# Kernel optimization log

Hardware: AMD Instinct MI355X
Metric: run time of the kernel (lower is better)

Reference implementation:

```python
import jax, jax.numpy as jnp
import numpy as np

B, S, D, H = 4, 2048, 1024, 16
HEAD = D // H
DENOM = float(np.sqrt(D))  # NOTE: original divides by sqrt(hidden_size), not sqrt(head_size)


def setup_inputs() -> dict:
    key = jax.random.key(0)
    ks = jax.random.split(key, 5)
    scale = 1.0 / np.sqrt(D)
    return {
        "hidden_state": jax.random.normal(ks[0], (B, S, D), dtype=jnp.float32),
        "attention_mask": jnp.ones((B, S), dtype=jnp.int32),  # unused in forward (faithful to source)
        "w_q": jax.random.normal(ks[1], (D, D), dtype=jnp.float32) * scale,
        "w_k": jax.random.normal(ks[2], (D, D), dtype=jnp.float32) * scale,
        "w_v": jax.random.normal(ks[3], (D, D), dtype=jnp.float32) * scale,
        "w_o": jax.random.normal(ks[4], (D, D), dtype=jnp.float32) * scale,
    }


def _split_heads(x):
    # [B, S, D] -> [B, H, S, head]
    b, s, _ = x.shape
    return x.reshape(b, s, H, HEAD).transpose(0, 2, 1, 3)


def reference(hidden_state, attention_mask, w_q, w_k, w_v, w_o):
    # nn.Linear(bias=False): y = x @ W^T with W of shape [out, in]
    q = _split_heads(hidden_state @ w_q.T)  # [B, H, S, head]
    k = _split_heads(hidden_state @ w_k.T)
    v = _split_heads(hidden_state @ w_v.T)
    qk = jnp.einsum("bhqd,bhkd->bhqk", q, k) / DENOM  # scale = 1/sqrt(hidden_size)
    attn = jax.nn.softmax(qk, axis=-1)  # attention_mask is NOT applied (matches source)
    ctx = jnp.einsum("bhqk,bhkd->bhqd", attn, v)  # [B, H, S, head]
    ctx = ctx.transpose(0, 2, 1, 3).reshape(hidden_state.shape[0], hidden_state.shape[1], D)
    return ctx @ w_o.T
```

## Files before the change

kernel.cpp:

```cpp
#include <hip/hip_runtime.h>
#include <hip/hip_bf16.h>
#include <math.h>

typedef __bf16 bf16x8 __attribute__((ext_vector_type(8)));
typedef __bf16 bf16x2 __attribute__((ext_vector_type(2)));
typedef float f32x4 __attribute__((ext_vector_type(4)));
typedef float f32x16 __attribute__((ext_vector_type(16)));
typedef unsigned u32x2v __attribute__((ext_vector_type(2)));
typedef unsigned u32x4v __attribute__((ext_vector_type(4)));
typedef unsigned short u16;

#define QSCALE 0.04508422002778011f

__device__ __forceinline__ u16 f2b(float f) {
  union { float f; unsigned u; } x; x.f = f;
  unsigned r = x.u + 0x7fffu + ((x.u >> 16) & 1u);
  return (u16)(r >> 16);
}

__device__ __forceinline__ unsigned pkbf(float a, float b) {
  bf16x2 t = { (__bf16)a, (__bf16)b };
  return __builtin_bit_cast(unsigned, t);
}

#define GLOAD_LDS16(g, s)                                                      \
  __builtin_amdgcn_global_load_lds(                                            \
      (__attribute__((address_space(1))) void*)(void*)(g),                     \
      (__attribute__((address_space(3))) void*)(s), 16, 0, 0)

__global__ void cast_all_kernel(const float* __restrict__ hs,
                                const float* __restrict__ wq, const float* __restrict__ wk,
                                const float* __restrict__ wv, const float* __restrict__ wo,
                                u16* __restrict__ hsb, u16* __restrict__ wqkv,
                                u16* __restrict__ wob) {
  const int w = blockIdx.y;
  const float* src; u16* dst; int n4; float scale = 1.0f;
  if (w == 0)      { src = hs; dst = hsb;                 n4 = 8192 * 1024 / 4; }
  else if (w == 1) { src = wq; dst = wqkv;                n4 = 1024 * 1024 / 4; scale = QSCALE; }
  else if (w == 2) { src = wk; dst = wqkv + 1024 * 1024;  n4 = 1024 * 1024 / 4; }
  else if (w == 3) { src = wv; dst = wqkv + 2 * 1024 * 1024; n4 = 1024 * 1024 / 4; }
  else             { src = wo; dst = wob;                 n4 = 1024 * 1024 / 4; }
  int i = blockIdx.x * blockDim.x + threadIdx.x;
  int stride = gridDim.x * blockDim.x;
  for (; i < n4; i += stride) {
    float4 v = ((const float4*)src)[i];
    ushort4 o;
    o.x = f2b(v.x * scale); o.y = f2b(v.y * scale);
    o.z = f2b(v.z * scale); o.w = f2b(v.w * scale);
    ((ushort4*)dst)[i] = o;
  }
}

template <int OUT_MODE>
__global__ __launch_bounds__(256) void gemm_nt64(const u16* __restrict__ A,
                                                 const u16* __restrict__ B,
                                                 void* __restrict__ O0,
                                                 u16* __restrict__ Ko,
                                                 u16* __restrict__ Vt,
                                                 int nbx) {
  __shared__ u16 As[128 * 64];
  __shared__ u16 Bs[128 * 64];
  const int tid = threadIdx.x;
  const int wid = tid >> 6, lane = tid & 63;
  const int fr = lane & 15, fg = lane >> 4;
  const int wr = wid >> 1, wc = wid & 1;
  const int id = blockIdx.x;
  const int cpx = gridDim.x >> 3;
  const int swzid = (id & 7) * cpx + (id >> 3);
  const int by = swzid / nbx, bx = swzid % nbx;
  const int m0 = by * 128, n0 = bx * 128;
  const int K = 1024;

  f32x4 acc[4][4] = {};

  for (int kt = 0; kt < K; kt += 64) {
#pragma unroll
    for (int i2 = 0; i2 < 4; ++i2) {
      int c = i2 * 256 + tid;
      int row = c >> 3, sl = c & 7;
      int kc = sl ^ (row & 7);
      GLOAD_LDS16(A + (size_t)(m0 + row) * K + kt + kc * 8, (char*)As + c * 16);
      GLOAD_LDS16(B + (size_t)(n0 + row) * K + kt + kc * 8, (char*)Bs + c * 16);
    }
    __syncthreads();

    bf16x8 af[4][2], bfr[4][2];
#pragma unroll
    for (int m = 0; m < 4; ++m) {
      const int row = wr * 64 + m * 16 + fr;
#pragma unroll
      for (int ks = 0; ks < 2; ++ks)
        af[m][ks] = *(const bf16x8*)((const char*)As + row * 128 +
                                     ((ks * 64 + fg * 16) ^ ((fr & 7) << 4)));
    }
#pragma unroll
    for (int n = 0; n < 4; ++n) {
      const int row = wc * 64 + n * 16 + fr;
#pragma unroll
      for (int ks = 0; ks < 2; ++ks)
        bfr[n][ks] = *(const bf16x8*)((const char*)Bs + row * 128 +
                                      ((ks * 64 + fg * 16) ^ ((fr & 7) << 4)));
    }
    __builtin_amdgcn_s_setprio(1);
#pragma unroll
    for (int m = 0; m < 4; ++m)
#pragma unroll
      for (int n = 0; n < 4; ++n)
#pragma unroll
        for (int ks = 0; ks < 2; ++ks)
          acc[m][n] = __builtin_amdgcn_mfma_f32_16x16x32_bf16(af[m][ks], bfr[n][ks],
                                                              acc[m][n], 0, 0, 0);
    __builtin_amdgcn_s_setprio(0);
    __syncthreads();
  }

#pragma unroll
  for (int m = 0; m < 4; ++m)
#pragma unroll
    for (int n = 0; n < 4; ++n) {
      int gr = m0 + wr * 64 + m * 16 + fg * 4;
      int gc = n0 + wc * 64 + n * 16 + fr;
      if (OUT_MODE == 0) {
#pragma unroll
        for (int j = 0; j < 4; ++j)
          ((float*)O0)[(size_t)(gr + j) * 1024 + gc] = acc[m][n][j];
      } else {
        const int region = n0 >> 10;
        if (region == 2) {
          int vc = gc - 2048;
          int hh = vc >> 6, dd = vc & 63, bb2 = gr >> 11, s0 = gr & 2047;
          ushort4 o;
          o.x = f2b(acc[m][n][0]); o.y = f2b(acc[m][n][1]);
          o.z = f2b(acc[m][n][2]); o.w = f2b(acc[m][n][3]);
          *(ushort4*)(Vt + (((size_t)bb2 * 16 + hh) * 64 + dd) * 2048 + s0) = o;
        } else {
          u16* dst = (region == 0) ? (u16*)O0 : Ko;
          int cc = gc & 1023;
#pragma unroll
          for (int j = 0; j < 4; ++j)
            dst[(size_t)(gr + j) * 1024 + cc] = f2b(acc[m][n][j]);
        }
      }
    }
}

__global__ __launch_bounds__(256, 2) void attn_fwd(const u16* __restrict__ Q,
                                                   const u16* __restrict__ Kg,
                                                   const u16* __restrict__ Vtg,
                                                   u16* __restrict__ O) {
  __shared__ u16 Ks[2][64 * 64];
  __shared__ u16 Vs[2][64 * 64];
  const int tid = threadIdx.x;
  const int wid = tid >> 6, lane = tid & 63;
  const int lq = lane & 31, hi = lane >> 5;
  const int id = blockIdx.x;
  const int swz = (id & 7) * 64 + (id >> 3);
  const int qb = swz & 7, bh = swz >> 3;
  const int b = bh >> 4, h = bh & 15;
  const size_t tokBase = (size_t)b * 2048 * 1024 + h * 64;
  const size_t vBase = (size_t)bh * 64 * 2048;
  const int q0 = qb * 256 + wid * 64;

  bf16x8 qfA[4], qfB[4];
#pragma unroll
  for (int s = 0; s < 4; ++s) {
    qfA[s] = *(const bf16x8*)(Q + tokBase + (size_t)(q0 + lq) * 1024 + s * 16 + hi * 8);
    qfB[s] = *(const bf16x8*)(Q + tokBase + (size_t)(q0 + 32 + lq) * 1024 + s * 16 + hi * 8);
  }

  f32x16 accA0 = {}, accA1 = {}, accB0 = {}, accB1 = {};
  f32x16 lsvA = {}, lsvB = {};

  const int skey = tid >> 3, sdc = tid & 7;
  const int sdg = sdc ^ (skey & 7);
  const int skey2 = (tid + 256) >> 3;
  const int sdg2 = sdc ^ (skey2 & 7);

#define STAGE(bb_, k0_) do {                                                          \
    GLOAD_LDS16(Kg + tokBase + (size_t)((k0_) + skey) * 1024 + sdg * 8,               \
                (char*)Ks[bb_] + tid * 16);                                           \
    GLOAD_LDS16(Kg + tokBase + (size_t)((k0_) + skey2) * 1024 + sdg2 * 8,             \
                (char*)Ks[bb_] + (tid + 256) * 16);                                   \
    GLOAD_LDS16(Vtg + vBase + (size_t)skey * 2048 + (k0_) + sdg * 8,                  \
                (char*)Vs[bb_] + tid * 16);                                           \
    GLOAD_LDS16(Vtg + vBase + (size_t)skey2 * 2048 + (k0_) + sdg2 * 8,                \
                (char*)Vs[bb_] + (tid + 256) * 16);                                   \
  } while (0)

  STAGE(0, 0);
  for (int t = 0; t < 32; ++t) {
    const int bb = t & 1;
    __syncthreads();
    if (t < 31) STAGE(bb ^ 1, (t + 1) * 64);

    f32x16 svA0 = {}, svA1 = {}, svB0 = {}, svB1 = {};
    __builtin_amdgcn_s_setprio(1);
#pragma unroll
    for (int s = 0; s < 4; ++s) {
      bf16x8 kf0 = *(const bf16x8*)((const char*)Ks[bb] + lq * 128 +
                                    ((s * 32 + hi * 16) ^ ((lq & 7) << 4)));
      bf16x8 kf1 = *(const bf16x8*)((const char*)Ks[bb] + (32 + lq) * 128 +
                                    ((s * 32 + hi * 16) ^ ((lq & 7) << 4)));
      svA0 = __builtin_amdgcn_mfma_f32_32x32x16_bf16(kf0, qfA[s], svA0, 0, 0, 0);
      svB0 = __builtin_amdgcn_mfma_f32_32x32x16_bf16(kf0, qfB[s], svB0, 0, 0, 0);
      svA1 = __builtin_amdgcn_mfma_f32_32x32x16_bf16(kf1, qfA[s], svA1, 0, 0, 0);
      svB1 = __builtin_amdgcn_mfma_f32_32x32x16_bf16(kf1, qfB[s], svB1, 0, 0, 0);
    }
    __builtin_amdgcn_s_setprio(0);

#pragma unroll
    for (int i = 0; i < 16; ++i) svA0[i] = __builtin_amdgcn_exp2f(svA0[i]);
#pragma unroll
    for (int i = 0; i < 16; ++i) svA1[i] = __builtin_amdgcn_exp2f(svA1[i]);
#pragma unroll
    for (int i = 0; i < 16; ++i) svB0[i] = __builtin_amdgcn_exp2f(svB0[i]);
#pragma unroll
    for (int i = 0; i < 16; ++i) svB1[i] = __builtin_amdgcn_exp2f(svB1[i]);
    lsvA += svA0; lsvA += svA1;
    lsvB += svB0; lsvB += svB1;

    bf16x8 paA[4], paB[4];
#pragma unroll
    for (int kb = 0; kb < 2; ++kb) {
#pragma unroll
      for (int hh = 0; hh < 2; ++hh) {
        const int rb = hh * 8;
        {
          const f32x16& pv = kb ? svA1 : svA0;
          unsigned w01 = pkbf(pv[rb + 0], pv[rb + 1]);
          unsigned w23 = pkbf(pv[rb + 2], pv[rb + 3]);
          unsigned w45 = pkbf(pv[rb + 4], pv[rb + 5]);
          unsigned w67 = pkbf(pv[rb + 6], pv[rb + 7]);
          u32x2v ra = __builtin_amdgcn_permlane32_swap(w01, w45, false, false);
          u32x2v rc = __builtin_amdgcn_permlane32_swap(w23, w67, false, false);
          u32x4v fw = { ra[0], rc[0], ra[1], rc[1] };
          paA[kb * 2 + hh] = __builtin_bit_cast(bf16x8, fw);
        }
        {
          const f32x16& pv = kb ? svB1 : svB0;
          unsigned w01 = pkbf(pv[rb + 0], pv[rb + 1]);
          unsigned w23 = pkbf(pv[rb + 2], pv[rb + 3]);
          unsigned w45 = pkbf(pv[rb + 4], pv[rb + 5]);
          unsigned w67 = pkbf(pv[rb + 6], pv[rb + 7]);
          u32x2v ra = __builtin_amdgcn_permlane32_swap(w01, w45, false, false);
          u32x2v rc = __builtin_amdgcn_permlane32_swap(w23, w67, false, false);
          u32x4v fw = { ra[0], rc[0], ra[1], rc[1] };
          paB[kb * 2 + hh] = __builtin_bit_cast(bf16x8, fw);
        }
      }
    }

    __builtin_amdgcn_s_setprio(1);
#pragma unroll
    for (int s = 0; s < 4; ++s) {
      bf16x8 bv0 = *(const bf16x8*)((const char*)Vs[bb] + lq * 128 +
                                    ((s * 32 + hi * 16) ^ ((lq & 7) << 4)));
      bf16x8 bv1 = *(const bf16x8*)((const char*)Vs[bb] + (32 + lq) * 128 +
                                    ((s * 32 + hi * 16) ^ ((lq & 7) << 4)));
      accA0 = __builtin_amdgcn_mfma_f32_32x32x16_bf16(paA[s], bv0, accA0, 0, 0, 0);
      accA1 = __builtin_amdgcn_mfma_f32_32x32x16_bf16(paA[s], bv1, accA1, 0, 0, 0);
      accB0 = __builtin_amdgcn_mfma_f32_32x32x16_bf16(paB[s], bv0, accB0, 0, 0, 0);
      accB1 = __builtin_amdgcn_mfma_f32_32x32x16_bf16(paB[s], bv1, accB1, 0, 0, 0);
    }
    __builtin_amdgcn_s_setprio(0);
  }
#undef STAGE

  float totA = 0.f, totB = 0.f;
#pragma unroll
  for (int i = 0; i < 16; ++i) { totA += lsvA[i]; totB += lsvB[i]; }
  totA += __shfl_xor(totA, 32);
  totB += __shfl_xor(totB, 32);
  const float invA = 1.0f / totA, invB = 1.0f / totB;
#pragma unroll
  for (int r = 0; r < 16; ++r) {
    const int q = (r & 3) + 8 * (r >> 2) + 4 * hi;
    const float ivA = __shfl(invA, q);
    const float ivB = __shfl(invB, q);
    const size_t rowA = (size_t)(b * 2048 + q0 + q) * 1024 + h * 64;
    const size_t rowB = (size_t)(b * 2048 + q0 + 32 + q) * 1024 + h * 64;
    O[rowA + lq]      = f2b(accA0[r] * ivA);
    O[rowA + 32 + lq] = f2b(accA1[r] * ivA);
    O[rowB + lq]      = f2b(accB0[r] * ivB);
    O[rowB + 32 + lq] = f2b(accB1[r] * ivB);
  }
}

extern "C" void kernel_launch(void* const* d_in, const int* in_sizes, int n_in,
                              void* d_out, int out_size, void* d_ws, size_t ws_size,
                              hipStream_t stream) {
  const float* hs = (const float*)d_in[0];
  const float* wq = (const float*)d_in[2];
  const float* wk = (const float*)d_in[3];
  const float* wv = (const float*)d_in[4];
  const float* wo = (const float*)d_in[5];

  const size_t TOK = 8192, DD = 1024;
  u16* hsb  = (u16*)d_ws;
  u16* wqkv = hsb + TOK * DD;
  u16* wob  = wqkv + 3 * DD * DD;
  u16* Qb   = wob + DD * DD;
  u16* Kb   = Qb + TOK * DD;
  u16* Vtg  = Kb + TOK * DD;
  u16* Cb   = Vtg + TOK * DD;

  cast_all_kernel<<<dim3(512, 5), 256, 0, stream>>>(hs, wq, wk, wv, wo, hsb, wqkv, wob);

  gemm_nt64<1><<<1536, 256, 0, stream>>>(hsb, wqkv, Qb, Kb, Vtg, 24);

  attn_fwd<<<dim3(512), 256, 0, stream>>>(Qb, Kb, Vtg, Cb);

  gemm_nt64<0><<<512, 256, 0, stream>>>(Cb, wob, d_out, nullptr, nullptr, 8);
}
```

Before: 189.3 us.

## Split attention over key halves with fp32 partials and a reduction kernel

Adds a split-K attention kernel that gives each block half of the key sequence. This doubles the grid to 1024 blocks and raises launch_bounds occupancy to 4, so more of the GPU is filled. Each half writes unnormalized fp32 partial accumulators and row sums to workspace, and a new reduce kernel adds them, normalizes, and writes bf16 context. This works without max-subtraction because the softmax is not max-shifted. The cost is about 64MB of extra fp32 traffic plus one more kernel launch, and the path falls back to the old kernel if the workspace is too small.

```diff
diff --git a/kernel.cpp b/kernel.cpp
--- a/kernel.cpp
+++ b/kernel.cpp
@@ -144,6 +144,82 @@
     }
 }
 
+#define ATTN_TILE_BODY(Kb_, Vb_)                                                      \
+    f32x16 svA0 = {}, svA1 = {}, svB0 = {}, svB1 = {};                                \
+    __builtin_amdgcn_s_setprio(1);                                                    \
+    _Pragma("unroll") for (int s = 0; s < 4; ++s) {                                   \
+      bf16x8 kf0 = *(const bf16x8*)((const char*)(Kb_) + lq * 128 +                   \
+                                    ((s * 32 + hi * 16) ^ ((lq & 7) << 4)));          \
+      bf16x8 kf1 = *(const bf16x8*)((const char*)(Kb_) + (32 + lq) * 128 +            \
+                                    ((s * 32 + hi * 16) ^ ((lq & 7) << 4)));          \
+      svA0 = __builtin_amdgcn_mfma_f32_32x32x16_bf16(kf0, qfA[s], svA0, 0, 0, 0);     \
+      svB0 = __builtin_amdgcn_mfma_f32_32x32x16_bf16(kf0, qfB[s], svB0, 0, 0, 0);     \
+      svA1 = __builtin_amdgcn_mfma_f32_32x32x16_bf16(kf1, qfA[s], svA1, 0, 0, 0);     \
+      svB1 = __builtin_amdgcn_mfma_f32_32x32x16_bf16(kf1, qfB[s], svB1, 0, 0, 0);     \
+    }                                                                                 \
+    __builtin_amdgcn_s_setprio(0);                                                    \
+    _Pragma("unroll") for (int i = 0; i < 16; ++i)                                    \
+      svA0[i] = __builtin_amdgcn_exp2f(svA0[i]);                                      \
+    _Pragma("unroll") for (int i = 0; i < 16; ++i)                                    \
+      svA1[i] = __builtin_amdgcn_exp2f(svA1[i]);                                      \
+    _Pragma("unroll") for (int i = 0; i < 16; ++i)                                    \
+      svB0[i] = __builtin_amdgcn_exp2f(svB0[i]);                                      \
+    _Pragma("unroll") for (int i = 0; i < 16; ++i)                                    \
+      svB1[i] = __builtin_amdgcn_exp2f(svB1[i]);                                      \
+    lsvA += svA0; lsvA += svA1;                                                       \
+    lsvB += svB0; lsvB += svB1;                                                       \
+    bf16x8 paA[4], paB[4];                                                            \
+    _Pragma("unroll") for (int kb = 0; kb < 2; ++kb) {                                \
+      _Pragma("unroll") for (int hh = 0; hh < 2; ++hh) {                              \
+        const int rb = hh * 8;                                                        \
+        {                                                                             \
+          const f32x16& pv = kb ? svA1 : svA0;                                        \
+          unsigned w01 = pkbf(pv[rb + 0], pv[rb + 1]);                                \
+          unsigned w23 = pkbf(pv[rb + 2], pv[rb + 3]);                                \
+          unsigned w45 = pkbf(pv[rb + 4], pv[rb + 5]);                                \
+          unsigned w67 = pkbf(pv[rb + 6], pv[rb + 7]);                                \
+          u32x2v ra = __builtin_amdgcn_permlane32_swap(w01, w45, false, false);       \
+          u32x2v rc = __builtin_amdgcn_permlane32_swap(w23, w67, false, false);       \
+          u32x4v fw = { ra[0], rc[0], ra[1], rc[1] };                                 \
+          paA[kb * 2 + hh] = __builtin_bit_cast(bf16x8, fw);                          \
+        }                                                                             \
+        {                                                                             \
+          const f32x16& pv = kb ? svB1 : svB0;                                        \
+          unsigned w01 = pkbf(pv[rb + 0], pv[rb + 1]);                                \
+          unsigned w23 = pkbf(pv[rb + 2], pv[rb + 3]);                                \
+          unsigned w45 = pkbf(pv[rb + 4], pv[rb + 5]);                                \
+          unsigned w67 = pkbf(pv[rb + 6], pv[rb + 7]);                                \
+          u32x2v ra = __builtin_amdgcn_permlane32_swap(w01, w45, false, false);       \
+          u32x2v rc = __builtin_amdgcn_permlane32_swap(w23, w67, false, false);       \
+          u32x4v fw = { ra[0], rc[0], ra[1], rc[1] };                                 \
+          paB[kb * 2 + hh] = __builtin_bit_cast(bf16x8, fw);                          \
+        }                                                                             \
+      }                                                                               \
+    }                                                                                 \
+    __builtin_amdgcn_s_setprio(1);                                                    \
+    _Pragma("unroll") for (int s = 0; s < 4; ++s) {                                   \
+      bf16x8 bv0 = *(const bf16x8*)((const char*)(Vb_) + lq * 128 +                   \
+                                    ((s * 32 + hi * 16) ^ ((lq & 7) << 4)));          \
+      bf16x8 bv1 = *(const bf16x8*)((const char*)(Vb_) + (32 + lq) * 128 +            \
+                                    ((s * 32 + hi * 16) ^ ((lq & 7) << 4)));          \
+      accA0 = __builtin_amdgcn_mfma_f32_32x32x16_bf16(paA[s], bv0, accA0, 0, 0, 0);   \
+      accA1 = __builtin_amdgcn_mfma_f32_32x32x16_bf16(paA[s], bv1, accA1, 0, 0, 0);   \
+      accB0 = __builtin_amdgcn_mfma_f32_32x32x16_bf16(paB[s], bv0, accB0, 0, 0, 0);   \
+      accB1 = __builtin_amdgcn_mfma_f32_32x32x16_bf16(paB[s], bv1, accB1, 0, 0, 0);   \
+    }                                                                                 \
+    __builtin_amdgcn_s_setprio(0);
+
+#define ATTN_STAGE(bb_, k0_) do {                                                     \
+    GLOAD_LDS16(Kg + tokBase + (size_t)((k0_) + skey) * 1024 + sdg * 8,               \
+                (char*)Ks[bb_] + tid * 16);                                           \
+    GLOAD_LDS16(Kg + tokBase + (size_t)((k0_) + skey2) * 1024 + sdg2 * 8,             \
+                (char*)Ks[bb_] + (tid + 256) * 16);                                   \
+    GLOAD_LDS16(Vtg + vBase + (size_t)skey * 2048 + (k0_) + sdg * 8,                  \
+                (char*)Vs[bb_] + tid * 16);                                           \
+    GLOAD_LDS16(Vtg + vBase + (size_t)skey2 * 2048 + (k0_) + sdg2 * 8,                \
+                (char*)Vs[bb_] + (tid + 256) * 16);                                   \
+  } while (0)
+
 __global__ __launch_bounds__(256, 2) void attn_fwd(const u16* __restrict__ Q,
                                                    const u16* __restrict__ Kg,
                                                    const u16* __restrict__ Vtg,
@@ -176,95 +252,13 @@
   const int skey2 = (tid + 256) >> 3;
   const int sdg2 = sdc ^ (skey2 & 7);
 
-#define STAGE(bb_, k0_) do {                                                          \
-    GLOAD_LDS16(Kg + tokBase + (size_t)((k0_) + skey) * 1024 + sdg * 8,               \
-                (char*)Ks[bb_] + tid * 16);                                           \
-    GLOAD_LDS16(Kg + tokBase + (size_t)((k0_) + skey2) * 1024 + sdg2 * 8,             \
-                (char*)Ks[bb_] + (tid + 256) * 16);                                   \
-    GLOAD_LDS16(Vtg + vBase + (size_t)skey * 2048 + (k0_) + sdg * 8,                  \
-                (char*)Vs[bb_] + tid * 16);                                           \
-    GLOAD_LDS16(Vtg + vBase + (size_t)skey2 * 2048 + (k0_) + sdg2 * 8,                \
-                (char*)Vs[bb_] + (tid + 256) * 16);                                   \
-  } while (0)
-
-  STAGE(0, 0);
+  ATTN_STAGE(0, 0);
   for (int t = 0; t < 32; ++t) {
     const int bb = t & 1;
     __syncthreads();
-    if (t < 31) STAGE(bb ^ 1, (t + 1) * 64);
-
-    f32x16 svA0 = {}, svA1 = {}, svB0 = {}, svB1 = {};
-    __builtin_amdgcn_s_setprio(1);
-#pragma unroll
-    for (int s = 0; s < 4; ++s) {
-      bf16x8 kf0 = *(const bf16x8*)((const char*)Ks[bb] + lq * 128 +
-                                    ((s * 32 + hi * 16) ^ ((lq & 7) << 4)));
-      bf16x8 kf1 = *(const bf16x8*)((const char*)Ks[bb] + (32 + lq) * 128 +
-                                    ((s * 32 + hi * 16) ^ ((lq & 7) << 4)));
-      svA0 = __builtin_amdgcn_mfma_f32_32x32x16_bf16(kf0, qfA[s], svA0, 0, 0, 0);
-      svB0 = __builtin_amdgcn_mfma_f32_32x32x16_bf16(kf0, qfB[s], svB0, 0, 0, 0);
-      svA1 = __builtin_amdgcn_mfma_f32_32x32x16_bf16(kf1, qfA[s], svA1, 0, 0, 0);
-      svB1 = __builtin_amdgcn_mfma_f32_32x32x16_bf16(kf1, qfB[s], svB1, 0, 0, 0);
-    }
-    __builtin_amdgcn_s_setprio(0);
-
-#pragma unroll
-    for (int i = 0; i < 16; ++i) svA0[i] = __builtin_amdgcn_exp2f(svA0[i]);
-#pragma unroll
-    for (int i = 0; i < 16; ++i) svA1[i] = __builtin_amdgcn_exp2f(svA1[i]);
-#pragma unroll
-    for (int i = 0; i < 16; ++i) svB0[i] = __builtin_amdgcn_exp2f(svB0[i]);
-#pragma unroll
-    for (int i = 0; i < 16; ++i) svB1[i] = __builtin_amdgcn_exp2f(svB1[i]);
-    lsvA += svA0; lsvA += svA1;
-    lsvB += svB0; lsvB += svB1;
-
-    bf16x8 paA[4], paB[4];
-#pragma unroll
-    for (int kb = 0; kb < 2; ++kb) {
-#pragma unroll
-      for (int hh = 0; hh < 2; ++hh) {
-        const int rb = hh * 8;
-        {
-          const f32x16& pv = kb ? svA1 : svA0;
-          unsigned w01 = pkbf(pv[rb + 0], pv[rb + 1]);
-          unsigned w23 = pkbf(pv[rb + 2], pv[rb + 3]);
-          unsigned w45 = pkbf(pv[rb + 4], pv[rb + 5]);
-          unsigned w67 = pkbf(pv[rb + 6], pv[rb + 7]);
-          u32x2v ra = __builtin_amdgcn_permlane32_swap(w01, w45, false, false);
-          u32x2v rc = __builtin_amdgcn_permlane32_swap(w23, w67, false, false);
-          u32x4v fw = { ra[0], rc[0], ra[1], rc[1] };
-          paA[kb * 2 + hh] = __builtin_bit_cast(bf16x8, fw);
-        }
-        {
-          const f32x16& pv = kb ? svB1 : svB0;
-          unsigned w01 = pkbf(pv[rb + 0], pv[rb + 1]);
-          unsigned w23 = pkbf(pv[rb + 2], pv[rb + 3]);
-          unsigned w45 = pkbf(pv[rb + 4], pv[rb + 5]);
-          unsigned w67 = pkbf(pv[rb + 6], pv[rb + 7]);
-          u32x2v ra = __builtin_amdgcn_permlane32_swap(w01, w45, false, false);
-          u32x2v rc = __builtin_amdgcn_permlane32_swap(w23, w67, false, false);
-          u32x4v fw = { ra[0], rc[0], ra[1], rc[1] };
-          paB[kb * 2 + hh] = __builtin_bit_cast(bf16x8, fw);
-        }
-      }
-    }
-
-    __builtin_amdgcn_s_setprio(1);
-#pragma unroll
-    for (int s = 0; s < 4; ++s) {
-      bf16x8 bv0 = *(const bf16x8*)((const char*)Vs[bb] + lq * 128 +
-                                    ((s * 32 + hi * 16) ^ ((lq & 7) << 4)));
-      bf16x8 bv1 = *(const bf16x8*)((const char*)Vs[bb] + (32 + lq) * 128 +
-                                    ((s * 32 + hi * 16) ^ ((lq & 7) << 4)));
-      accA0 = __builtin_amdgcn_mfma_f32_32x32x16_bf16(paA[s], bv0, accA0, 0, 0, 0);
-      accA1 = __builtin_amdgcn_mfma_f32_32x32x16_bf16(paA[s], bv1, accA1, 0, 0, 0);
-      accB0 = __builtin_amdgcn_mfma_f32_32x32x16_bf16(paB[s], bv0, accB0, 0, 0, 0);
-      accB1 = __builtin_amdgcn_mfma_f32_32x32x16_bf16(paB[s], bv1, accB1, 0, 0, 0);
-    }
-    __builtin_amdgcn_s_setprio(0);
-  }
-#undef STAGE
+    if (t < 31) ATTN_STAGE(bb ^ 1, (t + 1) * 64);
+    ATTN_TILE_BODY(Ks[bb], Vs[bb]);
+  }
 
   float totA = 0.f, totB = 0.f;
 #pragma unroll
@@ -286,6 +280,94 @@
   }
 }
 
+__global__ __launch_bounds__(256, 4) void attn_fwd_split(const u16* __restrict__ Q,
+                                                         const u16* __restrict__ Kg,
+                                                         const u16* __restrict__ Vtg,
+                                                         float* __restrict__ Pacc,
+                                                         float* __restrict__ Ptot) {
+  __shared__ u16 Ks[2][64 * 64];
+  __shared__ u16 Vs[2][64 * 64];
+  const int tid = threadIdx.x;
+  const int wid = tid >> 6, lane = tid & 63;
+  const int lq = lane & 31, hi = lane >> 5;
+  const int id = blockIdx.x;
+  const int swz = (id & 7) * 128 + (id >> 3);
+  const int kh = swz & 1, qb = (swz >> 1) & 7, bh = swz >> 4;
+  const int b = bh >> 4, h = bh & 15;
+  const size_t tokBase = (size_t)b * 2048 * 1024 + h * 64;
+  const size_t vBase = (size_t)bh * 64 * 2048;
+  const int q0 = qb * 256 + wid * 64;
+  const int kbase = kh * 1024;
+
+  bf16x8 qfA[4], qfB[4];
+#pragma unroll
+  for (int s = 0; s < 4; ++s) {
+    qfA[s] = *(const bf16x8*)(Q + tokBase + (size_t)(q0 + lq) * 1024 + s * 16 + hi * 8);
+    qfB[s] = *(const bf16x8*)(Q + tokBase + (size_t)(q0 + 32 + lq) * 1024 + s * 16 + hi * 8);
+  }
+
+  f32x16 accA0 = {}, accA1 = {}, accB0 = {}, accB1 = {};
+  f32x16 lsvA = {}, lsvB = {};
+
+  const int skey = tid >> 3, sdc = tid & 7;
+  const int sdg = sdc ^ (skey & 7);
+  const int skey2 = (tid + 256) >> 3;
+  const int sdg2 = sdc ^ (skey2 & 7);
+
+  ATTN_STAGE(0, kbase);
+  for (int t = 0; t < 16; ++t) {
+    const int bb = t & 1;
+    __syncthreads();
+    if (t < 15) ATTN_STAGE(bb ^ 1, kbase + (t + 1) * 64);
+    ATTN_TILE_BODY(Ks[bb], Vs[bb]);
+  }
+
+  float totA = 0.f, totB = 0.f;
+#pragma unroll
+  for (int i = 0; i < 16; ++i) { totA += lsvA[i]; totB += lsvB[i]; }
+  totA += __shfl_xor(totA, 32);
+  totB += __shfl_xor(totB, 32);
+
+  float* Pa = Pacc + (size_t)kh * 8192 * 1024;
+  if (hi == 0) {
+    float* Pt = Ptot + (size_t)kh * 64 * 2048 + (size_t)bh * 2048;
+    Pt[q0 + lq]      = totA;
+    Pt[q0 + 32 + lq] = totB;
+  }
+#pragma unroll
+  for (int r = 0; r < 16; ++r) {
+    const int q = (r & 3) + 8 * (r >> 2) + 4 * hi;
+    const size_t rowA = (size_t)(b * 2048 + q0 + q) * 1024 + h * 64;
+    const size_t rowB = (size_t)(b * 2048 + q0 + 32 + q) * 1024 + h * 64;
+    Pa[rowA + lq]      = accA0[r];
+    Pa[rowA + 32 + lq] = accA1[r];
+    Pa[rowB + lq]      = accB0[r];
+    Pa[rowB + 32 + lq] = accB1[r];
+  }
+}
+
+__global__ void reduce_split(const float* __restrict__ Pacc,
+                             const float* __restrict__ Ptot,
+                             u16* __restrict__ Cb) {
+  const int total = 8192 * 256;
+  int e = blockIdx.x * 256 + threadIdx.x;
+  for (; e < total; e += gridDim.x * 256) {
+    int tok = e >> 8, c4 = e & 255;
+    int h = (c4 * 4) >> 6;
+    int b = tok >> 11, s = tok & 2047;
+    int bh = b * 16 + h;
+    float4 p0 = ((const float4*)Pacc)[e];
+    float4 p1 = ((const float4*)(Pacc + (size_t)8192 * 1024))[e];
+    float t0 = Ptot[(size_t)bh * 2048 + s];
+    float t1 = Ptot[(size_t)64 * 2048 + (size_t)bh * 2048 + s];
+    float inv = 1.0f / (t0 + t1);
+    ushort4 o;
+    o.x = f2b((p0.x + p1.x) * inv); o.y = f2b((p0.y + p1.y) * inv);
+    o.z = f2b((p0.z + p1.z) * inv); o.w = f2b((p0.w + p1.w) * inv);
+    ((ushort4*)Cb)[e] = o;
+  }
+}
+
 extern "C" void kernel_launch(void* const* d_in, const int* in_sizes, int n_in,
                               void* d_out, int out_size, void* d_ws, size_t ws_size,
                               hipStream_t stream) {
@@ -303,12 +385,22 @@
   u16* Kb   = Qb + TOK * DD;
   u16* Vtg  = Kb + TOK * DD;
   u16* Cb   = Vtg + TOK * DD;
+  float* Pacc = (float*)(Cb + TOK * DD);
+  float* Ptot = Pacc + 2 * TOK * DD;
+
+  const size_t need = (size_t)(Cb + TOK * DD - hsb) * 2
+                    + (2 * TOK * DD + 2 * 64 * 2048) * 4;
 
   cast_all_kernel<<<dim3(512, 5), 256, 0, stream>>>(hs, wq, wk, wv, wo, hsb, wqkv, wob);
 
   gemm_nt64<1><<<1536, 256, 0, stream>>>(hsb, wqkv, Qb, Kb, Vtg, 24);
 
-  attn_fwd<<<dim3(512), 256, 0, stream>>>(Qb, Kb, Vtg, Cb);
+  if (ws_size >= need) {
+    attn_fwd_split<<<dim3(1024), 256, 0, stream>>>(Qb, Kb, Vtg, Pacc, Ptot);
+    reduce_split<<<2048, 256, 0, stream>>>(Pacc, Ptot, Cb);
+  } else {
+    attn_fwd<<<dim3(512), 256, 0, stream>>>(Qb, Kb, Vtg, Cb);
+  }
 
   gemm_nt64<0><<<512, 256, 0, stream>>>(Cb, wob, d_out, nullptr, nullptr, 8);
 }
```

Measured after the change: 733.2 us. 287% more time.
